# Optimization experiments

Hardware: AMD Instinct MI355X
Metric: run time of the kernel (lower is better)

Reference implementation:

```python
import jax, jax.numpy as jnp
import numpy as np

D_MODEL = 1024
DK = 64
H = D_MODEL // DK
EPS = 1e-5


def setup_inputs() -> dict:
    key = jax.random.key(0)
    ks = jax.random.split(key, 8)
    B, M = 4, 2048
    s = 1.0 / np.sqrt(D_MODEL)
    return {
        "inp": jax.random.normal(ks[0], (B, M, D_MODEL), dtype=jnp.float32),
        "Wq": jax.random.normal(ks[1], (D_MODEL, D_MODEL), dtype=jnp.float32) * s,
        "bq": jnp.zeros((D_MODEL,), dtype=jnp.float32),
        "Wk": jax.random.normal(ks[2], (D_MODEL, D_MODEL), dtype=jnp.float32) * s,
        "bk": jnp.zeros((D_MODEL,), dtype=jnp.float32),
        "Wv": jax.random.normal(ks[3], (D_MODEL, D_MODEL), dtype=jnp.float32) * s,
        "bv": jnp.zeros((D_MODEL,), dtype=jnp.float32),
        "gamma": jnp.ones((D_MODEL,), dtype=jnp.float32),
        "beta": jnp.zeros((D_MODEL,), dtype=jnp.float32),
    }


def reference(inp, Wq, bq, Wk, bk, Wv, bv, gamma, beta):
    B, M, _ = inp.shape
    # LayerNorm over last dim
    mu = jnp.mean(inp, axis=-1, keepdims=True)
    var = jnp.mean(jnp.square(inp - mu), axis=-1, keepdims=True)
    out = (inp - mu) * jax.lax.rsqrt(var + EPS) * gamma + beta
    # QKV projections (x @ W + b)
    Q = (out @ Wq + bq).reshape(B, M, DK, H)
    K = (out @ Wk + bk).reshape(B, M, DK, H)
    V = (out @ Wv + bv).reshape(B, M, DK, H)
    # per-position attention over the dk axis, contracting h
    scores = jnp.einsum("bmih,bmjh->bmij", Q, K) / np.sqrt(DK)  # [B,M,dk,dk]
    att = jax.nn.softmax(scores, axis=-1)
    res = jnp.einsum("bmij,bmjh->bmih", att, V).reshape(B, M, D_MODEL)
    # dropout is identity at eval; positionals add in original is dead code
    return inp + res
```

## Files before the change

### kernel.cpp

```cpp
#include <hip/hip_runtime.h>
#include <hip/hip_bf16.h>

#define D_MODEL 1024
#define NQKV 3072

typedef __attribute__((ext_vector_type(8))) short bf16x8;
typedef __attribute__((ext_vector_type(4))) float f32x4;
typedef __attribute__((ext_vector_type(16))) float f32x16;
typedef __attribute__((ext_vector_type(8))) unsigned short u16x8;

static __device__ __forceinline__ unsigned short f2bf(float f){
  unsigned int x = __float_as_uint(f);
  x += 0x7fff + ((x >> 16) & 1);
  return (unsigned short)(x >> 16);
}
static __device__ __forceinline__ float bf2f(unsigned short u){
  return __uint_as_float(((unsigned int)u) << 16);
}

__global__ __launch_bounds__(256) void ln_kernel(const float* __restrict__ inp,
    const float* __restrict__ gamma, const float* __restrict__ beta,
    unsigned short* __restrict__ X){
  const int row = blockIdx.x;
  const int t = threadIdx.x;
  const float4* ip = (const float4*)(inp + (size_t)row * D_MODEL);
  float4 v = ip[t];
  float s1 = v.x + v.y + v.z + v.w;
  float s2 = v.x*v.x + v.y*v.y + v.z*v.z + v.w*v.w;
#pragma unroll
  for (int off = 32; off >= 1; off >>= 1){
    s1 += __shfl_down(s1, off);
    s2 += __shfl_down(s2, off);
  }
  __shared__ float red[8];
  const int wave = t >> 6, lane = t & 63;
  if (lane == 0){ red[wave] = s1; red[4 + wave] = s2; }
  __syncthreads();
  s1 = red[0] + red[1] + red[2] + red[3];
  s2 = red[4] + red[5] + red[6] + red[7];
  const float mu   = s1 * (1.0f / D_MODEL);
  const float var  = s2 * (1.0f / D_MODEL) - mu * mu;
  const float rstd = rsqrtf(var + 1e-5f);
  float4 g = ((const float4*)gamma)[t];
  float4 b = ((const float4*)beta)[t];
  ushort4 o;
  o.x = f2bf((v.x - mu) * rstd * g.x + b.x);
  o.y = f2bf((v.y - mu) * rstd * g.y + b.y);
  o.z = f2bf((v.z - mu) * rstd * g.z + b.z);
  o.w = f2bf((v.w - mu) * rstd * g.w + b.w);
  ((ushort4*)(X + (size_t)row * D_MODEL))[t] = o;
}

__global__ __launch_bounds__(256) void wtrans_kernel(const float* __restrict__ Wq,
    const float* __restrict__ Wk, const float* __restrict__ Wv,
    const float* __restrict__ bq, const float* __restrict__ bk,
    const float* __restrict__ bv, unsigned short* __restrict__ Wt,
    float* __restrict__ bc){
  __shared__ float tile[32][33];
  const int z = blockIdx.z;
  const float* W = (z == 0) ? Wq : ((z == 1) ? Wk : Wv);
  const int k0 = blockIdx.x * 32, n0 = blockIdx.y * 32;
  const int r = threadIdx.x >> 5, c = threadIdx.x & 31;
  if (blockIdx.x == 0 && r == 0){
    const float* bsrc = (z == 0) ? bq : ((z == 1) ? bk : bv);
    bc[z * 1024 + n0 + c] = bsrc[n0 + c];
  }
#pragma unroll
  for (int i = 0; i < 4; i++)
    tile[r + i*8][c] = W[(size_t)(k0 + r + i*8) * D_MODEL + n0 + c];
  __syncthreads();
  unsigned short* dst = Wt + (size_t)(z * D_MODEL + n0) * D_MODEL + k0;
#pragma unroll
  for (int i = 0; i < 4; i++){
    int rr = r + i*8;
    dst[(size_t)rr * D_MODEL + c] = f2bf(tile[c][rr]);
  }
}


#define GLL(src, dst) __builtin_amdgcn_global_load_lds( \
    (const __attribute__((address_space(1))) void*)(src), \
    (__attribute__((address_space(3))) void*)(dst), 16, 0, 0)

#define STAGE(tsrc, bi) do { \
  const char* _sa = Ag + (size_t)r0*2048 + (size_t)(tsrc)*128 + co; \
  char* _da = ldsS + (size_t)(bi)*49152 + tid*16; \
  GLL(_sa, _da); GLL(_sa + 131072, _da + 8192); \
  const char* _sb = Bg + (size_t)r0*2048 + (size_t)(tsrc)*128 + co; \
  char* _db = ldsS + (size_t)(bi)*49152 + 16384 + tid*16; \
  GLL(_sb, _db); GLL(_sb + 131072, _db + 8192); \
  GLL(_sb + 262144, _db + 16384); GLL(_sb + 393216, _db + 24576); \
} while(0)

#define BODY(bi) do { \
  const char* Ab = ldsS + (size_t)(bi)*49152 + (wr*64 + lr)*128; \
  const char* Bb = ldsS + (size_t)(bi)*49152 + 16384 + (wc*64 + lr)*128; \
  bf16x8 Ar[4][2], Br[4][2]; \
  _Pragma("unroll") \
  for (int m = 0; m < 4; m++){ \
    Ar[m][0] = *(const bf16x8*)(Ab + m*2048 + colb0); \
    Ar[m][1] = *(const bf16x8*)(Ab + m*2048 + colb1); \
  } \
  _Pragma("unroll") \
  for (int n = 0; n < 4; n++){ \
    Br[n][0] = *(const bf16x8*)(Bb + n*2048 + colb0); \
    Br[n][1] = *(const bf16x8*)(Bb + n*2048 + colb1); \
  } \
  _Pragma("unroll") \
  for (int m = 0; m < 4; m++) \
    _Pragma("unroll") \
    for (int n = 0; n < 4; n++){ \
      acc[m][n] = __builtin_amdgcn_mfma_f32_16x16x32_bf16(Ar[m][0], Br[n][0], acc[m][n], 0, 0, 0); \
      acc[m][n] = __builtin_amdgcn_mfma_f32_16x16x32_bf16(Ar[m][1], Br[n][1], acc[m][n], 0, 0, 0); \
    } \
} while(0)

#define BARRIER __builtin_amdgcn_s_barrier()
#define SCHEDB  __builtin_amdgcn_sched_barrier(0)
#define VMCNT6  asm volatile("s_waitcnt vmcnt(6)" ::: "memory")
#define VMCNT0  asm volatile("s_waitcnt vmcnt(0)" ::: "memory")

__global__ __launch_bounds__(512, 2) void gemm128x256_kernel(const unsigned short* __restrict__ A,
    const unsigned short* __restrict__ Bt, const float* __restrict__ bias,
    unsigned short* __restrict__ C){
  __shared__ __align__(16) char ldsS[3 * 49152];
  const int tid = threadIdx.x;
  const int wave = tid >> 6, lane = tid & 63;
  const int wr = wave >> 2, wc = wave & 3;
  const int lr = lane & 15;
  const int colb0 = ((lane >> 4) * 16) ^ ((lane & 7) << 4);
  const int colb1 = (64 + (lane >> 4) * 16) ^ ((lane & 7) << 4);

  const int b = blockIdx.x;
  const int xcd = b & 7;
  const int i = b >> 3;
  const int mi = i & 7, ni = i >> 3;
  const int m0 = (xcd * 8 + mi) * 128;
  const int n0 = ni * 256;

  const int r0 = tid >> 3;
  const size_t co = (size_t)(((tid & 7) * 16) ^ ((r0 & 7) << 4));
  const char* Ag = (const char*)(A + (size_t)m0 * 1024);
  const char* Bg = (const char*)(Bt + (size_t)n0 * 1024);

  f32x4 acc[4][4] = {};

  STAGE(0, 0);
  STAGE(1, 1);
  VMCNT6; BARRIER; SCHEDB;

  for (int t = 0; t < 16; ++t){
    if (t <= 13) STAGE(t + 2, (t + 2) % 3);
    BODY(t % 3);
    if (t <= 13)      { SCHEDB; VMCNT6; BARRIER; SCHEDB; }
    else if (t == 14) { SCHEDB; VMCNT0; BARRIER; SCHEDB; }
  }

  const int gm = m0 + wr*64;
  const int gn = n0 + wc*64;
  const int rr0 = (lane >> 4) * 4;
#pragma unroll
  for (int nf = 0; nf < 4; nf++){
    const int gcol = gn + nf*16 + lr;
    const float bb = bias[gcol];
#pragma unroll
    for (int mf = 0; mf < 4; mf++){
      const int grow = gm + mf*16 + rr0;
#pragma unroll
      for (int r = 0; r < 4; r++)
        C[(size_t)(grow + r) * NQKV + gcol] = f2bf(acc[mf][nf][r] + bb);
    }
  }
}

__global__ __launch_bounds__(256) void attn_kernel(const unsigned short* __restrict__ qkv,
    const float* __restrict__ inp, float* __restrict__ out){
  __shared__ unsigned short P[4][64 * 64];
  const int wave = threadIdx.x >> 6, lane = threadIdx.x & 63;
  const int token = blockIdx.x * 4 + wave;
  const unsigned short* row = qkv + (size_t)token * NQKV;
  const int l31 = lane & 31, hi = lane >> 5;
  const int l15 = lane & 15, qg = lane >> 4;
  char* pbase = (char*)&P[wave][0];

  bf16x8 kf[2], qf[2];
#pragma unroll
  for (int mt = 0; mt < 2; mt++)
    kf[mt] = *(const bf16x8*)(row + 1024 + (mt*32 + l31)*16 + hi*8);
#pragma unroll
  for (int nt = 0; nt < 2; nt++)
    qf[nt] = *(const bf16x8*)(row + (nt*32 + l31)*16 + hi*8);

  bf16x8 vf[2];
#pragma unroll
  for (int kc = 0; kc < 2; kc++)
#pragma unroll
    for (int e = 0; e < 8; e++)
      vf[kc][e] = (short)row[2048 + (kc*32 + qg*8 + e)*16 + l15];

  f32x16 s[2][2] = {};
#pragma unroll
  for (int mt = 0; mt < 2; mt++)
#pragma unroll
    for (int nt = 0; nt < 2; nt++)
      s[mt][nt] = __builtin_amdgcn_mfma_f32_32x32x16_bf16(kf[mt], qf[nt], s[mt][nt], 0, 0, 0);

#pragma unroll
  for (int ti = 0; ti < 2; ti++){
    float m = s[0][ti][0];
#pragma unroll
    for (int mt = 0; mt < 2; mt++)
#pragma unroll
      for (int r = 0; r < 16; r++) m = fmaxf(m, s[mt][ti][r]);
    m = fmaxf(m, __shfl_xor(m, 32));
    float sum = 0.0f;
#pragma unroll
    for (int mt = 0; mt < 2; mt++)
#pragma unroll
      for (int r = 0; r < 16; r++){
        float p = exp2f((s[mt][ti][r] - m) * 0.1803368801f);
        s[mt][ti][r] = p;
        sum += p;
      }
    sum += __shfl_xor(sum, 32);
    const float invs = 1.0f / sum;
    const int i = ti*32 + l31;
    const int sw = (i & 7) << 4;
#pragma unroll
    for (int mt = 0; mt < 2; mt++)
#pragma unroll
      for (int g = 0; g < 4; g++){
        ushort4 pk;
        pk.x = f2bf(s[mt][ti][4*g + 0] * invs);
        pk.y = f2bf(s[mt][ti][4*g + 1] * invs);
        pk.z = f2bf(s[mt][ti][4*g + 2] * invs);
        pk.w = f2bf(s[mt][ti][4*g + 3] * invs);
        const int jbyte = mt*64 + g*16 + hi*8;
        *(ushort4*)(pbase + ((i*128 + jbyte) ^ sw)) = pk;
      }
  }
  __syncthreads();

  f32x4 o[4] = {};
#pragma unroll
  for (int nt = 0; nt < 4; nt++){
    const int n = nt*16 + l15;
    const int swr = (n & 7) << 4;
#pragma unroll
    for (int kc = 0; kc < 2; kc++){
      bf16x8 pb = *(const bf16x8*)(pbase + ((n*128 + kc*64 + qg*16) ^ swr));
      o[nt] = __builtin_amdgcn_mfma_f32_16x16x32_bf16(vf[kc], pb, o[nt], 0, 0, 0);
    }
  }

  const size_t base = (size_t)token * D_MODEL;
#pragma unroll
  for (int nt = 0; nt < 4; nt++){
    const int i = nt*16 + l15;
    const float4 iv = *(const float4*)(inp + base + i*16 + qg*4);
    float4 ov;
    ov.x = iv.x + o[nt][0];
    ov.y = iv.y + o[nt][1];
    ov.z = iv.z + o[nt][2];
    ov.w = iv.w + o[nt][3];
    *(float4*)(out + base + i*16 + qg*4) = ov;
  }
}

extern "C" void kernel_launch(void* const* d_in, const int* in_sizes, int n_in,
                              void* d_out, int out_size, void* d_ws, size_t ws_size,
                              hipStream_t stream) {
  const float* inp   = (const float*)d_in[0];
  const float* Wq    = (const float*)d_in[1];
  const float* bq    = (const float*)d_in[2];
  const float* Wk    = (const float*)d_in[3];
  const float* bk    = (const float*)d_in[4];
  const float* Wv    = (const float*)d_in[5];
  const float* bv    = (const float*)d_in[6];
  const float* gamma = (const float*)d_in[7];
  const float* beta  = (const float*)d_in[8];
  float* out = (float*)d_out;

  char* ws = (char*)d_ws;
  unsigned short* Xln  = (unsigned short*)ws;
  unsigned short* Wt   = (unsigned short*)(ws + 16777216);
  float*          bc   = (float*)(ws + 23068672);
  unsigned short* QKV  = (unsigned short*)(ws + 23080960);

  ln_kernel<<<8192, 256, 0, stream>>>(inp, gamma, beta, Xln);
  wtrans_kernel<<<dim3(32, 32, 3), 256, 0, stream>>>(Wq, Wk, Wv, bq, bk, bv, Wt, bc);
  gemm128x256_kernel<<<768, 512, 0, stream>>>(Xln, Wt, bc, QKV);
  attn_kernel<<<2048, 256, 0, stream>>>(QKV, inp, out);
}
```

Measured before the change: 96.51 us.

## Split GEMM K-step into two phases interleaving loads, barriers and prioritized MFMAs

Each K tile in the QKV GEMM main loop now runs as two half-phases. Each half reads one column half of the A and B fragments from LDS, issues part of the next tile's global-to-LDS loads, then runs 16 MFMAs under raised wave priority (s_setprio). The goal is to overlap LDS reads and global loads with matrix math and to halve fragment register use. The cost is more barriers per iteration and explicit lgkmcnt waits, which may stall waves more often.

```diff
diff --git a/kernel.cpp b/kernel.cpp
--- a/kernel.cpp
+++ b/kernel.cpp
@@ -82,43 +82,46 @@
     (const __attribute__((address_space(1))) void*)(src), \
     (__attribute__((address_space(3))) void*)(dst), 16, 0, 0)
 
-#define STAGE(tsrc, bi) do { \
+#define STAGE_P0(tsrc, bi) do { \
   const char* _sa = Ag + (size_t)r0*2048 + (size_t)(tsrc)*128 + co; \
   char* _da = ldsS + (size_t)(bi)*49152 + tid*16; \
   GLL(_sa, _da); GLL(_sa + 131072, _da + 8192); \
   const char* _sb = Bg + (size_t)r0*2048 + (size_t)(tsrc)*128 + co; \
   char* _db = ldsS + (size_t)(bi)*49152 + 16384 + tid*16; \
-  GLL(_sb, _db); GLL(_sb + 131072, _db + 8192); \
+  GLL(_sb, _db); \
+} while(0)
+
+#define STAGE_P1(tsrc, bi) do { \
+  const char* _sb = Bg + (size_t)r0*2048 + (size_t)(tsrc)*128 + co; \
+  char* _db = ldsS + (size_t)(bi)*49152 + 16384 + tid*16; \
+  GLL(_sb + 131072, _db + 8192); \
   GLL(_sb + 262144, _db + 16384); GLL(_sb + 393216, _db + 24576); \
 } while(0)
 
-#define BODY(bi) do { \
+#define PHASE_READS(bi, cb) do { \
   const char* Ab = ldsS + (size_t)(bi)*49152 + (wr*64 + lr)*128; \
   const char* Bb = ldsS + (size_t)(bi)*49152 + 16384 + (wc*64 + lr)*128; \
-  bf16x8 Ar[4][2], Br[4][2]; \
   _Pragma("unroll") \
-  for (int m = 0; m < 4; m++){ \
-    Ar[m][0] = *(const bf16x8*)(Ab + m*2048 + colb0); \
-    Ar[m][1] = *(const bf16x8*)(Ab + m*2048 + colb1); \
-  } \
+  for (int m = 0; m < 4; m++) Ar[m] = *(const bf16x8*)(Ab + m*2048 + (cb)); \
   _Pragma("unroll") \
-  for (int n = 0; n < 4; n++){ \
-    Br[n][0] = *(const bf16x8*)(Bb + n*2048 + colb0); \
-    Br[n][1] = *(const bf16x8*)(Bb + n*2048 + colb1); \
-  } \
+  for (int n = 0; n < 4; n++) Br[n] = *(const bf16x8*)(Bb + n*2048 + (cb)); \
+} while(0)
+
+#define PHASE_MFMA do { \
+  __builtin_amdgcn_s_setprio(1); \
   _Pragma("unroll") \
   for (int m = 0; m < 4; m++) \
     _Pragma("unroll") \
-    for (int n = 0; n < 4; n++){ \
-      acc[m][n] = __builtin_amdgcn_mfma_f32_16x16x32_bf16(Ar[m][0], Br[n][0], acc[m][n], 0, 0, 0); \
-      acc[m][n] = __builtin_amdgcn_mfma_f32_16x16x32_bf16(Ar[m][1], Br[n][1], acc[m][n], 0, 0, 0); \
-    } \
+    for (int n = 0; n < 4; n++) \
+      acc[m][n] = __builtin_amdgcn_mfma_f32_16x16x32_bf16(Ar[m], Br[n], acc[m][n], 0, 0, 0); \
+  __builtin_amdgcn_s_setprio(0); \
 } while(0)
 
 #define BARRIER __builtin_amdgcn_s_barrier()
 #define SCHEDB  __builtin_amdgcn_sched_barrier(0)
 #define VMCNT6  asm volatile("s_waitcnt vmcnt(6)" ::: "memory")
 #define VMCNT0  asm volatile("s_waitcnt vmcnt(0)" ::: "memory")
+#define LGKM0   asm volatile("s_waitcnt lgkmcnt(0)" ::: "memory")
 
 __global__ __launch_bounds__(512, 2) void gemm128x256_kernel(const unsigned short* __restrict__ A,
     const unsigned short* __restrict__ Bt, const float* __restrict__ bias,
@@ -144,16 +147,29 @@
   const char* Bg = (const char*)(Bt + (size_t)n0 * 1024);
 
   f32x4 acc[4][4] = {};
-
-  STAGE(0, 0);
-  STAGE(1, 1);
+  bf16x8 Ar[4], Br[4];
+
+  STAGE_P0(0, 0); STAGE_P1(0, 0);
+  STAGE_P0(1, 1); STAGE_P1(1, 1);
   VMCNT6; BARRIER; SCHEDB;
 
   for (int t = 0; t < 16; ++t){
-    if (t <= 13) STAGE(t + 2, (t + 2) % 3);
-    BODY(t % 3);
-    if (t <= 13)      { SCHEDB; VMCNT6; BARRIER; SCHEDB; }
-    else if (t == 14) { SCHEDB; VMCNT0; BARRIER; SCHEDB; }
+    const int buf = t % 3;
+    const int nbuf = (t + 2) % 3;
+    PHASE_READS(buf, colb0);
+    if (t <= 13) STAGE_P0(t + 2, nbuf);
+    BARRIER;
+    LGKM0; SCHEDB;
+    PHASE_MFMA;
+    BARRIER; SCHEDB;
+    PHASE_READS(buf, colb1);
+    if (t <= 13) STAGE_P1(t + 2, nbuf);
+    if (t <= 13)      { SCHEDB; VMCNT6; }
+    else if (t == 14) { SCHEDB; VMCNT0; }
+    BARRIER;
+    LGKM0; SCHEDB;
+    PHASE_MFMA;
+    if (t < 15) { BARRIER; SCHEDB; }
   }
 
   const int gm = m0 + wr*64;
```

Measured after the change: 98.28 us. Within noise of the previous version (+1.8%).
